# Kernel optimization log

Measured on AMD Instinct MI355X. Metric: run time of the kernel, lower is better.

The kernel has to match this reference:

```python
import jax, jax.numpy as jnp
import numpy as np

E = 50000      # entity_total
R = 100        # relation_total
DIM = 128      # config.dim
M = 10         # max_context_num
M1 = M + 1
T = 2 * R + 2  # entity_gcn_weight rows (2R+1) + appended zero row
B = 1024


def setup_inputs() -> dict:
    key = jax.random.key(0)
    ks = jax.random.split(key, 40)
    f = jnp.float32
    stdv = 1.0 / np.sqrt(DIM)
    inp = {}
    inp['entity_emb'] = jax.random.normal(ks[0], (E, DIM), f) * 0.05
    inp['relation_emb'] = jax.random.normal(ks[1], (R, DIM), f) * 0.05
    ec = jax.random.normal(ks[2], (E + 1, DIM), f) * 0.05
    inp['entity_context'] = ec.at[E].set(0.0)   # padding_idx row = 0
    rc = jax.random.normal(ks[3], (R + 1, DIM), f) * 0.05
    inp['relation_context'] = rc.at[R].set(0.0)
    inp['entity_gcn_weight'] = jax.random.uniform(ks[4], (2 * R + 1, DIM, DIM), f, -stdv, stdv)
    inp['relation_gcn_weight'] = jax.random.uniform(ks[5], (DIM, DIM), f, -stdv, stdv)
    inp['gate_entity'] = jax.random.uniform(ks[6], (DIM,), f)
    inp['gate_relation'] = jax.random.uniform(ks[7], (DIM,), f)
    inp['v_ent'] = jax.random.uniform(ks[8], (DIM,), f)
    inp['v_rel'] = jax.random.uniform(ks[9], (DIM,), f)
    inp['pos_h'] = jax.random.randint(ks[10], (B,), 0, E)
    inp['pos_r'] = jax.random.randint(ks[11], (B,), 0, R)
    inp['pos_t'] = jax.random.randint(ks[12], (B,), 0, E)
    inp['neg_h'] = jax.random.randint(ks[13], (B,), 0, E)
    inp['neg_r'] = jax.random.randint(ks[14], (B,), 0, R)
    inp['neg_t'] = jax.random.randint(ks[15], (B,), 0, E)
    inp['ph_adj'] = jax.random.randint(ks[16], (B, M), 0, E + 1)
    inp['pt_adj'] = jax.random.randint(ks[17], (B, M), 0, E + 1)
    inp['nh_adj'] = jax.random.randint(ks[18], (B, M), 0, E + 1)
    inp['nt_adj'] = jax.random.randint(ks[19], (B, M), 0, E + 1)
    inp['pr_adj'] = jax.random.randint(ks[20], (B, M, 2), 0, R + 1)
    inp['nr_adj'] = jax.random.randint(ks[21], (B, M, 2), 0, R + 1)
    inp['ph_R'] = jax.random.randint(ks[22], (B, M1, M1), 0, T)
    inp['pt_R'] = jax.random.randint(ks[23], (B, M1, M1), 0, T)
    inp['nh_R'] = jax.random.randint(ks[24], (B, M1, M1), 0, T)
    inp['nt_R'] = jax.random.randint(ks[25], (B, M1, M1), 0, T)
    inp['ph_nn'] = jax.random.randint(ks[26], (B,), 0, M)
    inp['pt_nn'] = jax.random.randint(ks[27], (B,), 0, M)
    inp['nh_nn'] = jax.random.randint(ks[28], (B,), 0, M)
    inp['nt_nn'] = jax.random.randint(ks[29], (B,), 0, M)
    inp['ph_D'] = jax.random.uniform(ks[30], (B, M1, M1), f)
    inp['pt_D'] = jax.random.uniform(ks[31], (B, M1, M1), f)
    inp['nh_D'] = jax.random.uniform(ks[32], (B, M1, M1), f)
    inp['nt_D'] = jax.random.uniform(ks[33], (B, M1, M1), f)
    inp['pr_A'] = jax.random.normal(ks[34], (B, M1, M1), f)
    inp['nr_A'] = jax.random.normal(ks[35], (B, M1, M1), f)
    return inp


def reference(entity_emb, relation_emb, entity_context, relation_context,
              entity_gcn_weight, relation_gcn_weight, gate_entity, gate_relation,
              v_ent, v_rel,
              pos_h, pos_r, pos_t, neg_h, neg_r, neg_t,
              ph_adj, pt_adj, nh_adj, nt_adj, pr_adj, nr_adj,
              ph_R, pt_R, nh_R, nt_R, ph_nn, pt_nn, nh_nn, nt_nn,
              ph_D, pt_D, nh_D, nt_D, pr_A, nr_A):
    # weight table with trailing zero row (padding relation type T-1)
    Wfull = jnp.concatenate(
        [entity_gcn_weight, jnp.zeros((1, DIM, DIM), entity_gcn_weight.dtype)], axis=0)

    def ent_ctx(vec, adj_idx):
        # center vector + M gathered context vectors -> [B, M1, d]
        return jnp.concatenate([vec[:, None, :], entity_context[adj_idx]], axis=1)

    def rel_ctx(vec, adj_idx):
        # relation context comes in (head,tail) pairs, summed over the 2
        a = relation_context[adj_idx].sum(axis=2)  # [B, M, d]
        return jnp.concatenate([vec[:, None, :], a], axis=1)

    def rgcn(Rt, Dm, nn_, H):
        # vectorized R-GCN: out[b,j] = relu(sum_k D[b,j,k] * H[b,j] @ W[Rt[b,j,k]])
        # restricted to the dynamic (n+1)x(n+1) block via masking.
        j = jnp.arange(M1)
        valid = j[None, :] <= nn_[:, None]                 # [B, M1]
        pair = valid[:, :, None] & valid[:, None, :]       # [B, M1, M1]
        Rm = jnp.where(pair, Rt, T - 1)                    # pad -> zero weight
        Dd = jnp.where(pair, Dm, jnp.zeros((), Dm.dtype))
        # segment-reduce D over relation types: C[b,j,t] = sum_{k: Rm=t} D[b,j,k]
        C = (jax.nn.one_hot(Rm, T, dtype=H.dtype) * Dd[..., None]).sum(axis=2)  # [B,M1,T]
        S = jnp.einsum('bjt,tde->bjde', C, Wfull)          # [B, M1, d, d]
        out = jax.nn.relu(jnp.einsum('bjd,bjde->bje', H, S))
        return jnp.where(valid[..., None], out, jnp.zeros((), out.dtype))

    def gcn_rel(A, H):
        return jax.nn.relu(jnp.einsum('bij,bjd,de->bie', A, H, relation_gcn_weight))

    def subgraph(o, adj, v):
        # attention over context rows, then weighted sum
        tmp = jax.nn.relu(adj * o[:, None, :])             # [B, M1, d]
        alpha = jax.nn.softmax(tmp @ v, axis=1)            # [B, M1]
        return jnp.sum(alpha[..., None] * adj, axis=1)     # [B, d]

    p_h = entity_emb[pos_h]; p_t = entity_emb[pos_t]; p_r = relation_emb[pos_r]
    n_h = entity_emb[neg_h]; n_t = entity_emb[neg_t]; n_r = relation_emb[neg_r]

    ph_v = rgcn(ph_R, ph_D, ph_nn, ent_ctx(p_h, ph_adj))
    pt_v = rgcn(pt_R, pt_D, pt_nn, ent_ctx(p_t, pt_adj))
    nh_v = rgcn(nh_R, nh_D, nh_nn, ent_ctx(n_h, nh_adj))
    nt_v = rgcn(nt_R, nt_D, nt_nn, ent_ctx(n_t, nt_adj))
    pr_v = gcn_rel(pr_A, rel_ctx(p_r, pr_adj))
    nr_v = gcn_rel(nr_A, rel_ctx(n_r, nr_adj))

    ph_sg = subgraph(p_h, ph_v, v_ent); pt_sg = subgraph(p_t, pt_v, v_ent)
    nh_sg = subgraph(n_h, nh_v, v_ent); nt_sg = subgraph(n_t, nt_v, v_ent)
    pr_sg = subgraph(p_r, pr_v, v_rel); nr_sg = subgraph(n_r, nr_v, v_rel)

    ge = jax.nn.sigmoid(gate_entity)
    gr = jax.nn.sigmoid(gate_relation)
    ph_o = ge * p_h + (1 - ge) * ph_sg
    pt_o = ge * p_t + (1 - ge) * pt_sg
    nh_o = ge * n_h + (1 - ge) * nh_sg
    nt_o = ge * n_t + (1 - ge) * nt_sg
    pr_o = gr * p_r + (1 - gr) * pr_sg
    nr_o = gr * n_r + (1 - gr) * nr_sg

    p_score = jnp.linalg.norm(ph_o + pr_o - pt_o, ord=2, axis=1)
    n_score = jnp.linalg.norm(nh_o + nr_o - nt_o, ord=2, axis=1)
    return (p_score, n_score)
```

## Files before the change

### kernel.cpp

```cpp
#include <hip/hip_runtime.h>
#include <math.h>

#define B_   1024
#define M_   10
#define M1_  11
#define DIM_ 128
#define NW_  201
#define NQUAD_ (4*B_*M1_*M1_)
#define IPB_  64
#define SLOTS_ 2048
#define SCATB_ 242
#define WTILES_ ((NW_+1)*16)
#define MAXCHK_ (NW_ + NQUAD_/IPB_)

typedef __attribute__((ext_vector_type(8))) short bf16x8;
typedef __attribute__((ext_vector_type(4))) float f32x4;

struct GatherPtrs {
    const int* center[4];
    const int* adj[4];
    const int* nn[4];
    const int* Rt[4];
    const float* Dm[4];
};

struct RelPtrs {
    const int* center[2];
    const int* adj2[2];
    const float* A[2];
};

__device__ __forceinline__ unsigned short f2bf(float f) {
    union { float f; unsigned u; } v; v.f = f;
    const unsigned r = v.u + 0x7FFFu + ((v.u >> 16) & 1u);
    return (unsigned short)(r >> 16);
}

template <int N>
__device__ __forceinline__ void block_reduce_bcast(float (&p)[N], float (*sred)[N],
                                                   int e, float (&sc)[N])
{
    #pragma unroll
    for (int off = 32; off; off >>= 1)
        #pragma unroll
        for (int i = 0; i < N; ++i) p[i] += __shfl_xor(p[i], off, 64);
    __syncthreads();
    if ((e & 63) == 0) {
        #pragma unroll
        for (int i = 0; i < N; ++i) sred[e >> 6][i] = p[i];
    }
    __syncthreads();
    #pragma unroll
    for (int i = 0; i < N; ++i) sc[i] = sred[0][i] + sred[1][i];
}

__device__ __forceinline__ float attn_pool(const float (&vm)[M1_], float o, float ve,
                                           float (*sred)[M1_], int e)
{
    float p[M1_];
    #pragma unroll
    for (int j = 0; j < M1_; ++j) p[j] = fmaxf(vm[j] * o, 0.f) * ve;
    float sc[M1_];
    block_reduce_bcast<M1_>(p, sred, e, sc);
    float mx = sc[0];
    #pragma unroll
    for (int j = 1; j < M1_; ++j) mx = fmaxf(mx, sc[j]);
    float s = 0.f, ex[M1_];
    #pragma unroll
    for (int j = 0; j < M1_; ++j) { ex[j] = expf(sc[j] - mx); s += ex[j]; }
    const float inv = 1.f / s;
    float sg = 0.f;
    #pragma unroll
    for (int j = 0; j < M1_; ++j) sg += ex[j] * inv * vm[j];
    return sg;
}

__global__ __launch_bounds__(256)
void prep_kernel(GatherPtrs gp,
                 const float* __restrict__ W, const float* __restrict__ Wr,
                 unsigned short* __restrict__ WT,
                 int* __restrict__ cursor,
                 int2* __restrict__ itemsEQ, float* __restrict__ itemsD)
{
    __shared__ int lh[NW_];
    __shared__ int lbase[NW_];
    __shared__ float tile[32][33];
    const int tid = threadIdx.x;
    const int bid = blockIdx.x;

    if (bid < SCATB_) {
        if (tid < NW_) lh[tid] = 0;
        __syncthreads();
        int rr[8], rk[8], ei[8], qv[8];
        float dv[8];
        #pragma unroll
        for (int s = 0; s < 8; ++s) {
            const int idx = bid * 2048 + s * 256 + tid;
            const int c = idx / (B_ * M1_ * M1_);
            const int rem = idx % (B_ * M1_ * M1_);
            const int b = rem / (M1_ * M1_);
            const int jk = rem % (M1_ * M1_);
            const int j = jk / M1_, k = jk % M1_;
            const int n = gp.nn[c][b];
            rr[s] = -1;
            if (j <= n && k <= n) {
                const int r = gp.Rt[c][rem];
                if (r < NW_) {
                    rr[s] = r;
                    rk[s] = atomicAdd(&lh[r], 1);
                    const int eidx = (j == 0) ? gp.center[c][b]
                                              : gp.adj[c][b * M_ + (j - 1)];
                    ei[s] = (eidx << 1) | (j != 0);
                    qv[s] = idx;
                    dv[s] = gp.Dm[c][rem];
                }
            }
        }
        __syncthreads();
        if (tid < NW_) lbase[tid] = lh[tid] ? atomicAdd(&cursor[tid], lh[tid]) : 0;
        __syncthreads();
        #pragma unroll
        for (int s = 0; s < 8; ++s)
            if (rr[s] >= 0) {
                const int slot = lbase[rr[s]] + rk[s];
                if (slot < SLOTS_) {
                    itemsEQ[rr[s] * SLOTS_ + slot] = make_int2(ei[s], qv[s]);
                    itemsD[rr[s] * SLOTS_ + slot] = dv[s];
                }
            }
    } else {
        const int tl = bid - SCATB_;
        const int t = tl >> 4, sub = tl & 15;
        const int bd = (sub >> 2) * 32, be = (sub & 3) * 32;
        const float* Ws = (t < NW_) ? (W + (size_t)t * DIM_ * DIM_) : Wr;
        unsigned short* Wd = WT + (size_t)t * DIM_ * DIM_;
        const int tx = tid & 31, ty = tid >> 5;
        #pragma unroll
        for (int r = 0; r < 32; r += 8)
            tile[r + ty][tx] = Ws[(bd + r + ty) * DIM_ + be + tx];
        __syncthreads();
        #pragma unroll
        for (int r = 0; r < 32; r += 8)
            Wd[(be + r + ty) * DIM_ + bd + tx] = f2bf(tile[tx][r + ty]);
    }
}

__global__ __launch_bounds__(256)
void chunkbuild_kernel(const int* __restrict__ cursor,
                       int* __restrict__ chunkTab, int* __restrict__ nchunks)
{
    __shared__ int nch[NW_];
    __shared__ int bs[NW_ + 1];
    const int t = threadIdx.x;
    if (t < NW_) {
        const int cnt = min(cursor[t], SLOTS_);
        nch[t] = (cnt + IPB_ - 1) >> 6;
    }
    __syncthreads();
    if (t == 0) {
        int acc = 0;
        for (int i = 0; i < NW_; ++i) { bs[i] = acc; acc += nch[i]; }
        bs[NW_] = acc;
        nchunks[0] = acc;
    }
    __syncthreads();
    if (t < NW_)
        for (int c = 0; c < nch[t]; ++c) chunkTab[bs[t] + c] = (t << 16) | c;
}

template <bool FAST>
__global__ __launch_bounds__(256)
void rgcn_gemm(const float* __restrict__ ent_emb,
               const float* __restrict__ ent_ctx,
               const unsigned short* __restrict__ WT,
               const int2* __restrict__ itemsEQ,
               const float* __restrict__ itemsD,
               const int* __restrict__ cursor,
               const int* __restrict__ chunkTab,
               const int* __restrict__ nchunks,
               _Float16* __restrict__ partial,
               float* __restrict__ vent)
{
    __shared__ unsigned short sH[IPB_ * DIM_];
    __shared__ int sQ[IPB_];
    __shared__ float sD[IPB_];

    const int bid = blockIdx.x;
    if (bid >= nchunks[0]) return;
    const int ent = chunkTab[bid];
    const int t = ent >> 16, ch = ent & 0xffff;
    const int cnt = min(cursor[t], SLOTS_);
    const int istart = ch * IPB_;
    const int nItems = min(IPB_, cnt - istart);
    const int tid = threadIdx.x;
    const int2* eqBase = itemsEQ + t * SLOTS_ + istart;

    #pragma unroll
    for (int it4 = 0; it4 < 4; ++it4) {
        const int m = it4 * 256 + tid;
        const int it = m >> 4, chd = m & 15;
        uint4 pkd;
        if (it < nItems) {
            const int2 eq = eqBase[it];
            if (chd == 0) {
                sQ[it] = eq.y;
                sD[it] = itemsD[t * SLOTS_ + istart + it];
            }
            const float* srow = (eq.x & 1)
                ? ent_ctx + (size_t)(eq.x >> 1) * DIM_
                : ent_emb + (size_t)(eq.x >> 1) * DIM_;
            const float4* s4 = (const float4*)srow + chd * 2;
            const float4 v0 = s4[0], v1 = s4[1];
            pkd.x = (unsigned)f2bf(v0.x) | ((unsigned)f2bf(v0.y) << 16);
            pkd.y = (unsigned)f2bf(v0.z) | ((unsigned)f2bf(v0.w) << 16);
            pkd.z = (unsigned)f2bf(v1.x) | ((unsigned)f2bf(v1.y) << 16);
            pkd.w = (unsigned)f2bf(v1.z) | ((unsigned)f2bf(v1.w) << 16);
        } else {
            if (chd == 0) { sQ[it] = -1; sD[it] = 0.f; }
            pkd.x = pkd.y = pkd.z = pkd.w = 0u;
        }
        const int so = it * 256 + ((chd * 16) ^ ((it & 7) << 4));
        *reinterpret_cast<uint4*>(reinterpret_cast<char*>(sH) + so) = pkd;
    }
    __syncthreads();

    const int w = tid >> 6, l = tid & 63;
    const int lr = l & 15, lk = l >> 4;
    const unsigned short* Wp = WT + (size_t)t * DIM_ * DIM_;
    const f32x4 z = {0.f, 0.f, 0.f, 0.f};
    f32x4 acc[4][2];
    #pragma unroll
    for (int mi = 0; mi < 4; ++mi) { acc[mi][0] = z; acc[mi][1] = z; }

    #pragma unroll
    for (int kb = 0; kb < 4; ++kb) {
        const int o = kb * 64 + lk * 16;
        bf16x8 af[4], bfr[2];
        #pragma unroll
        for (int ni = 0; ni < 2; ++ni) {
            const int row = (2 * w + ni) * 16 + lr;
            bfr[ni] = *reinterpret_cast<const bf16x8*>(Wp + (size_t)row * DIM_ + kb * 32 + lk * 8);
        }
        #pragma unroll
        for (int mi = 0; mi < 4; ++mi) {
            const int row = mi * 16 + lr;
            af[mi] = *reinterpret_cast<const bf16x8*>(
                reinterpret_cast<const char*>(sH) + row * 256 + (o ^ ((row & 7) << 4)));
        }
        #pragma unroll
        for (int mi = 0; mi < 4; ++mi)
            #pragma unroll
            for (int ni = 0; ni < 2; ++ni)
                acc[mi][ni] = __builtin_amdgcn_mfma_f32_16x16x32_bf16(
                    af[mi], bfr[ni], acc[mi][ni], 0, 0, 0);
    }

    #pragma unroll
    for (int mi = 0; mi < 4; ++mi) {
        #pragma unroll
        for (int jj = 0; jj < 4; ++jj) {
            const int it = mi * 16 + lk * 4 + jj;
            const int q = sQ[it];
            if (q >= 0) {
                const float d = sD[it];
                #pragma unroll
                for (int ni = 0; ni < 2; ++ni) {
                    const int col = (2 * w + ni) * 16 + lr;
                    const float val = acc[mi][ni][jj] * d;
                    if (FAST) {
                        partial[(size_t)q * DIM_ + col] = (_Float16)val;
                    } else {
                        unsafeAtomicAdd(vent + (size_t)(q / M1_) * DIM_ + col, val);
                    }
                }
            }
        }
    }
}

template <bool FAST>
__global__ __launch_bounds__(128)
void pool_kernel(GatherPtrs gp, RelPtrs rp,
                 const float* __restrict__ ent_emb,
                 const float* __restrict__ rel_emb,
                 const float* __restrict__ rel_ctx,
                 const unsigned short* __restrict__ WT,
                 const float* __restrict__ v_ent,
                 const float* __restrict__ v_rel,
                 const _Float16* __restrict__ partial,
                 const float* __restrict__ vent,
                 float* __restrict__ sgbuf)
{
    __shared__ float sred[2][M1_];
    const int b = blockIdx.x, c = blockIdx.y, e = threadIdx.x;

    if (c < 4) {
        __shared__ int sRt[M1_ * M1_];
        const int n = gp.nn[c][b];
        if (FAST && e < M1_ * M1_) sRt[e] = gp.Rt[c][b * (M1_ * M1_) + e];
        __syncthreads();

        const float o = ent_emb[(size_t)gp.center[c][b] * DIM_ + e];
        float vm[M1_];
        if (FAST) {
            #pragma unroll
            for (int j = 0; j < M1_; ++j) {
                float s = 0.f;
                if (j <= n) {
                    const int base = (c * B_ + b) * (M1_ * M1_) + j * M1_;
                    #pragma unroll
                    for (int k = 0; k < M1_; ++k) {
                        const float v = (float)partial[(size_t)(base + k) * DIM_ + e];
                        s += (k <= n && sRt[j * M1_ + k] < NW_) ? v : 0.f;
                    }
                    s = fmaxf(s, 0.f);
                }
                vm[j] = s;
            }
        } else {
            const float* vmat = vent + ((size_t)(c * B_ + b)) * M1_ * DIM_;
            #pragma unroll
            for (int j = 0; j < M1_; ++j)
                vm[j] = (j <= n) ? fmaxf(vmat[j * DIM_ + e], 0.f) : 0.f;
        }
        const float sg = attn_pool(vm, o, v_ent[e], sred, e);
        sgbuf[((size_t)c * B_ + b) * DIM_ + e] = sg;
    } else {
        __shared__ float sA[M1_ * M1_];
        __shared__ unsigned short sAH[16 * DIM_];
        __shared__ float sOut[M1_][DIM_];
        const int cse = c - 4;
        const int* adj2 = rp.adj2[cse];

        float h[M1_];
        const float o = rel_emb[(size_t)rp.center[cse][b] * DIM_ + e];
        h[0] = o;
        #pragma unroll
        for (int j = 1; j < M1_; ++j) {
            const int a0 = adj2[((b * M_) + (j - 1)) * 2 + 0];
            const int a1 = adj2[((b * M_) + (j - 1)) * 2 + 1];
            h[j] = rel_ctx[(size_t)a0 * DIM_ + e] + rel_ctx[(size_t)a1 * DIM_ + e];
        }
        if (e < M1_ * M1_) sA[e] = rp.A[cse][b * (M1_ * M1_) + e];
        __syncthreads();

        #pragma unroll
        for (int i = 0; i < M1_; ++i) {
            float s = 0.f;
            #pragma unroll
            for (int jj = 0; jj < M1_; ++jj) s += sA[i * M1_ + jj] * h[jj];
            *reinterpret_cast<unsigned short*>(
                reinterpret_cast<char*>(sAH) + i * 256 + ((2 * e) ^ ((i & 7) << 4))) = f2bf(s);
        }
        #pragma unroll
        for (int i = M1_; i < 16; ++i)
            *reinterpret_cast<unsigned short*>(
                reinterpret_cast<char*>(sAH) + i * 256 + ((2 * e) ^ ((i & 7) << 4))) = 0;
        __syncthreads();

        const int w = e >> 6, l = e & 63;
        const int lr = l & 15, lk = l >> 4;
        const unsigned short* WrT = WT + (size_t)NW_ * DIM_ * DIM_;
        const f32x4 z = {0.f, 0.f, 0.f, 0.f};
        f32x4 acc[4] = {z, z, z, z};
        #pragma unroll
        for (int kb = 0; kb < 4; ++kb) {
            const bf16x8 af = *reinterpret_cast<const bf16x8*>(
                reinterpret_cast<const char*>(sAH) + lr * 256 + ((kb * 64 + lk * 16) ^ ((lr & 7) << 4)));
            #pragma unroll
            for (int ni = 0; ni < 4; ++ni) {
                const int cb = w * 4 + ni;
                const bf16x8 bfr = *reinterpret_cast<const bf16x8*>(
                    WrT + (size_t)(cb * 16 + lr) * DIM_ + kb * 32 + lk * 8);
                acc[ni] = __builtin_amdgcn_mfma_f32_16x16x32_bf16(af, bfr, acc[ni], 0, 0, 0);
            }
        }
        #pragma unroll
        for (int ni = 0; ni < 4; ++ni) {
            const int col = (w * 4 + ni) * 16 + lr;
            #pragma unroll
            for (int jj = 0; jj < 4; ++jj) {
                const int i = lk * 4 + jj;
                if (i < M1_) sOut[i][col] = fmaxf(acc[ni][jj], 0.f);
            }
        }
        __syncthreads();

        float vm[M1_];
        #pragma unroll
        for (int i = 0; i < M1_; ++i) vm[i] = sOut[i][e];
        const float sg = attn_pool(vm, o, v_rel[e], sred, e);
        sgbuf[((size_t)c * B_ + b) * DIM_ + e] = sg;
    }
}

__global__ __launch_bounds__(128)
void score_kernel(GatherPtrs gp,
                  const float* __restrict__ ent_emb,
                  const float* __restrict__ rel_emb,
                  const int* __restrict__ pos_r, const int* __restrict__ neg_r,
                  const float* __restrict__ gate_e, const float* __restrict__ gate_r,
                  const float* __restrict__ sgbuf,
                  float* __restrict__ out)
{
    __shared__ float sred[2][2];
    const int b = blockIdx.x, e = threadIdx.x;

    float cvec[4], osg[4];
    #pragma unroll
    for (int c = 0; c < 4; ++c) {
        cvec[c] = ent_emb[(size_t)gp.center[c][b] * DIM_ + e];
        osg[c] = sgbuf[((size_t)c * B_ + b) * DIM_ + e];
    }
    const float rvec0 = rel_emb[(size_t)pos_r[b] * DIM_ + e];
    const float rvec1 = rel_emb[(size_t)neg_r[b] * DIM_ + e];
    const float rsg0 = sgbuf[((size_t)4 * B_ + b) * DIM_ + e];
    const float rsg1 = sgbuf[((size_t)5 * B_ + b) * DIM_ + e];

    const float ge = 1.f / (1.f + expf(-gate_e[e]));
    const float gr = 1.f / (1.f + expf(-gate_r[e]));
    const float ph_o = ge * cvec[0] + (1.f - ge) * osg[0];
    const float pt_o = ge * cvec[1] + (1.f - ge) * osg[1];
    const float nh_o = ge * cvec[2] + (1.f - ge) * osg[2];
    const float nt_o = ge * cvec[3] + (1.f - ge) * osg[3];
    const float pr_o = gr * rvec0 + (1.f - gr) * rsg0;
    const float nr_o = gr * rvec1 + (1.f - gr) * rsg1;

    const float pv = ph_o + pr_o - pt_o;
    const float nv = nh_o + nr_o - nt_o;
    float p2[2] = { pv * pv, nv * nv };
    float sc2[2];
    block_reduce_bcast<2>(p2, sred, e, sc2);
    if (e == 0) { out[b] = sqrtf(sc2[0]); out[B_ + b] = sqrtf(sc2[1]); }
}

extern "C" void kernel_launch(void* const* d_in, const int* in_sizes, int n_in,
                              void* d_out, int out_size, void* d_ws, size_t ws_size,
                              hipStream_t stream)
{
    const float* entity_emb   = (const float*)d_in[0];
    const float* relation_emb = (const float*)d_in[1];
    const float* entity_ctx   = (const float*)d_in[2];
    const float* relation_ctx = (const float*)d_in[3];
    const float* egw          = (const float*)d_in[4];
    const float* rgw          = (const float*)d_in[5];
    const float* gate_e       = (const float*)d_in[6];
    const float* gate_r       = (const float*)d_in[7];
    const float* v_ent        = (const float*)d_in[8];
    const float* v_rel        = (const float*)d_in[9];
    const int* pos_h = (const int*)d_in[10];
    const int* pos_r = (const int*)d_in[11];
    const int* pos_t = (const int*)d_in[12];
    const int* neg_h = (const int*)d_in[13];
    const int* neg_r = (const int*)d_in[14];
    const int* neg_t = (const int*)d_in[15];
    const int* ph_adj = (const int*)d_in[16];
    const int* pt_adj = (const int*)d_in[17];
    const int* nh_adj = (const int*)d_in[18];
    const int* nt_adj = (const int*)d_in[19];
    const int* pr_adj = (const int*)d_in[20];
    const int* nr_adj = (const int*)d_in[21];
    const int* ph_R = (const int*)d_in[22];
    const int* pt_R = (const int*)d_in[23];
    const int* nh_R = (const int*)d_in[24];
    const int* nt_R = (const int*)d_in[25];
    const int* ph_nn = (const int*)d_in[26];
    const int* pt_nn = (const int*)d_in[27];
    const int* nh_nn = (const int*)d_in[28];
    const int* nt_nn = (const int*)d_in[29];
    const float* ph_D = (const float*)d_in[30];
    const float* pt_D = (const float*)d_in[31];
    const float* nh_D = (const float*)d_in[32];
    const float* nt_D = (const float*)d_in[33];
    const float* pr_A = (const float*)d_in[34];
    const float* nr_A = (const float*)d_in[35];

    GatherPtrs gp;
    gp.center[0] = pos_h; gp.center[1] = pos_t; gp.center[2] = neg_h; gp.center[3] = neg_t;
    gp.adj[0] = ph_adj; gp.adj[1] = pt_adj; gp.adj[2] = nh_adj; gp.adj[3] = nt_adj;
    gp.nn[0] = ph_nn; gp.nn[1] = pt_nn; gp.nn[2] = nh_nn; gp.nn[3] = nt_nn;
    gp.Rt[0] = ph_R; gp.Rt[1] = pt_R; gp.Rt[2] = nh_R; gp.Rt[3] = nt_R;
    gp.Dm[0] = ph_D; gp.Dm[1] = pt_D; gp.Dm[2] = nh_D; gp.Dm[3] = nt_D;

    RelPtrs rp;
    rp.center[0] = pos_r; rp.center[1] = neg_r;
    rp.adj2[0] = pr_adj; rp.adj2[1] = nr_adj;
    rp.A[0] = pr_A; rp.A[1] = nr_A;

    char* wsb = (char*)d_ws;
    const size_t partialBytes = (size_t)NQUAD_ * DIM_ * 2;
    const size_t eqBytes      = (size_t)NW_ * SLOTS_ * 8;
    const size_t dBytes       = (size_t)NW_ * SLOTS_ * 4;
    const size_t metaBytes    = 65536;
    const size_t wtBytes      = (size_t)(NW_ + 1) * DIM_ * DIM_ * 2;
    const size_t sgBytes      = (size_t)6 * B_ * DIM_ * 4;
    const size_t fastNeed = partialBytes + eqBytes + dBytes + metaBytes + wtBytes;
    const bool fast = (ws_size >= fastNeed);

    if (fast) {
        _Float16* partial = (_Float16*)wsb;
        int2* itemsEQ = (int2*)(wsb + partialBytes);
        float* itemsD = (float*)(wsb + partialBytes + eqBytes);
        char* meta    = wsb + partialBytes + eqBytes + dBytes;
        int* cursor   = (int*)meta;
        int* nchunks  = (int*)(meta + 1024);
        int* chunkTab = (int*)(meta + 2048);
        char* wsg = wsb + partialBytes + eqBytes + dBytes + metaBytes;
        unsigned short* WT = (unsigned short*)wsg;
        float* sgbuf       = (float*)wsg;

        hipMemsetAsync(cursor, 0, 1024, stream);
        prep_kernel<<<dim3(SCATB_ + WTILES_), dim3(256), 0, stream>>>(
            gp, egw, rgw, WT, cursor, itemsEQ, itemsD);
        chunkbuild_kernel<<<dim3(1), dim3(256), 0, stream>>>(cursor, chunkTab, nchunks);
        rgcn_gemm<true><<<dim3(MAXCHK_), dim3(256), 0, stream>>>(
            entity_emb, entity_ctx, WT, itemsEQ, itemsD, cursor, chunkTab, nchunks,
            partial, nullptr);
        pool_kernel<true><<<dim3(B_, 6), dim3(128), 0, stream>>>(
            gp, rp, entity_emb, relation_emb, relation_ctx, WT,
            v_ent, v_rel, partial, nullptr, sgbuf);
        score_kernel<<<dim3(B_), dim3(128), 0, stream>>>(
            gp, entity_emb, relation_emb, pos_r, neg_r, gate_e, gate_r, sgbuf, (float*)d_out);
    } else {
        float* vent = (float*)wsb;
        const size_t ventBytes = (size_t)4 * B_ * M1_ * DIM_ * 4;
        unsigned short* WT = (unsigned short*)(wsb + ventBytes);
        float* sgbuf  = (float*)(wsb + ventBytes + wtBytes);
        int2* itemsEQ = (int2*)(wsb + ventBytes + wtBytes + sgBytes);
        float* itemsD = (float*)(wsb + ventBytes + wtBytes + sgBytes + eqBytes);
        char* meta    = wsb + ventBytes + wtBytes + sgBytes + eqBytes + dBytes;
        int* cursor   = (int*)meta;
        int* nchunks  = (int*)(meta + 1024);
        int* chunkTab = (int*)(meta + 2048);

        hipMemsetAsync(vent, 0, ventBytes, stream);
        hipMemsetAsync(cursor, 0, 1024, stream);
        prep_kernel<<<dim3(SCATB_ + WTILES_), dim3(256), 0, stream>>>(
            gp, egw, rgw, WT, cursor, itemsEQ, itemsD);
        chunkbuild_kernel<<<dim3(1), dim3(256), 0, stream>>>(cursor, chunkTab, nchunks);
        rgcn_gemm<false><<<dim3(MAXCHK_), dim3(256), 0, stream>>>(
            entity_emb, entity_ctx, WT, itemsEQ, itemsD, cursor, chunkTab, nchunks,
            nullptr, vent);
        pool_kernel<false><<<dim3(B_, 6), dim3(128), 0, stream>>>(
            gp, rp, entity_emb, relation_emb, relation_ctx, WT,
            v_ent, v_rel, nullptr, vent, sgbuf);
        score_kernel<<<dim3(B_), dim3(128), 0, stream>>>(
            gp, entity_emb, relation_emb, pos_r, neg_r, gate_e, gate_r, sgbuf, (float*)d_out);
    }
}
```

Before: 95.78 us.

## Fuse chunk build into prep via last-block pattern and merge pool with score

Removes the single-block chunkbuild launch. The last scatter block of prep_kernel, detected through an atomic done counter placed in the memset region, now builds the chunk table. pool_kernel and score_kernel are merged into one 768-thread epi_kernel per batch row, so the sg intermediate stays in shared memory and the global sgbuf round trip plus one launch go away. The cost is a larger block with more shared memory, which may lower occupancy, plus a threadfence and atomic in the scatter blocks.

New measurement: 151.1 us. +57.8%, slower.

```diff
diff --git a/kernel.cpp b/kernel.cpp
--- a/kernel.cpp
+++ b/kernel.cpp
@@ -36,55 +36,20 @@
     return (unsigned short)(r >> 16);
 }
 
-template <int N>
-__device__ __forceinline__ void block_reduce_bcast(float (&p)[N], float (*sred)[N],
-                                                   int e, float (&sc)[N])
-{
-    #pragma unroll
-    for (int off = 32; off; off >>= 1)
-        #pragma unroll
-        for (int i = 0; i < N; ++i) p[i] += __shfl_xor(p[i], off, 64);
-    __syncthreads();
-    if ((e & 63) == 0) {
-        #pragma unroll
-        for (int i = 0; i < N; ++i) sred[e >> 6][i] = p[i];
-    }
-    __syncthreads();
-    #pragma unroll
-    for (int i = 0; i < N; ++i) sc[i] = sred[0][i] + sred[1][i];
-}
-
-__device__ __forceinline__ float attn_pool(const float (&vm)[M1_], float o, float ve,
-                                           float (*sred)[M1_], int e)
-{
-    float p[M1_];
-    #pragma unroll
-    for (int j = 0; j < M1_; ++j) p[j] = fmaxf(vm[j] * o, 0.f) * ve;
-    float sc[M1_];
-    block_reduce_bcast<M1_>(p, sred, e, sc);
-    float mx = sc[0];
-    #pragma unroll
-    for (int j = 1; j < M1_; ++j) mx = fmaxf(mx, sc[j]);
-    float s = 0.f, ex[M1_];
-    #pragma unroll
-    for (int j = 0; j < M1_; ++j) { ex[j] = expf(sc[j] - mx); s += ex[j]; }
-    const float inv = 1.f / s;
-    float sg = 0.f;
-    #pragma unroll
-    for (int j = 0; j < M1_; ++j) sg += ex[j] * inv * vm[j];
-    return sg;
-}
-
 __global__ __launch_bounds__(256)
 void prep_kernel(GatherPtrs gp,
                  const float* __restrict__ W, const float* __restrict__ Wr,
                  unsigned short* __restrict__ WT,
-                 int* __restrict__ cursor,
-                 int2* __restrict__ itemsEQ, float* __restrict__ itemsD)
+                 int* __restrict__ cursor, int* __restrict__ done,
+                 int2* __restrict__ itemsEQ, float* __restrict__ itemsD,
+                 int* __restrict__ chunkTab, int* __restrict__ nchunks)
 {
     __shared__ int lh[NW_];
     __shared__ int lbase[NW_];
     __shared__ float tile[32][33];
+    __shared__ int sLast;
+    __shared__ int nchS[NW_];
+    __shared__ int bsS[NW_ + 1];
     const int tid = threadIdx.x;
     const int bid = blockIdx.x;
 
@@ -128,6 +93,26 @@
                     itemsD[rr[s] * SLOTS_ + slot] = dv[s];
                 }
             }
+        __threadfence();
+        __syncthreads();
+        if (tid == 0) sLast = (atomicAdd(done, 1) == SCATB_ - 1);
+        __syncthreads();
+        if (sLast) {
+            if (tid < NW_) {
+                const int cnt = min(atomicAdd(&cursor[tid], 0), SLOTS_);
+                nchS[tid] = (cnt + IPB_ - 1) >> 6;
+            }
+            __syncthreads();
+            if (tid == 0) {
+                int acc = 0;
+                for (int i = 0; i < NW_; ++i) { bsS[i] = acc; acc += nchS[i]; }
+                nchunks[0] = acc;
+            }
+            __syncthreads();
+            if (tid < NW_)
+                for (int c = 0; c < nchS[tid]; ++c)
+                    chunkTab[bsS[tid] + c] = (tid << 16) | c;
+        }
     } else {
         const int tl = bid - SCATB_;
         const int t = tl >> 4, sub = tl & 15;
@@ -143,29 +128,6 @@
         for (int r = 0; r < 32; r += 8)
             Wd[(be + r + ty) * DIM_ + bd + tx] = f2bf(tile[tx][r + ty]);
     }
-}
-
-__global__ __launch_bounds__(256)
-void chunkbuild_kernel(const int* __restrict__ cursor,
-                       int* __restrict__ chunkTab, int* __restrict__ nchunks)
-{
-    __shared__ int nch[NW_];
-    __shared__ int bs[NW_ + 1];
-    const int t = threadIdx.x;
-    if (t < NW_) {
-        const int cnt = min(cursor[t], SLOTS_);
-        nch[t] = (cnt + IPB_ - 1) >> 6;
-    }
-    __syncthreads();
-    if (t == 0) {
-        int acc = 0;
-        for (int i = 0; i < NW_; ++i) { bs[i] = acc; acc += nch[i]; }
-        bs[NW_] = acc;
-        nchunks[0] = acc;
-    }
-    __syncthreads();
-    if (t < NW_)
-        for (int c = 0; c < nch[t]; ++c) chunkTab[bs[t] + c] = (t << 16) | c;
 }
 
 template <bool FAST>
@@ -279,85 +241,98 @@
 }
 
 template <bool FAST>
-__global__ __launch_bounds__(128)
-void pool_kernel(GatherPtrs gp, RelPtrs rp,
-                 const float* __restrict__ ent_emb,
-                 const float* __restrict__ rel_emb,
-                 const float* __restrict__ rel_ctx,
-                 const unsigned short* __restrict__ WT,
-                 const float* __restrict__ v_ent,
-                 const float* __restrict__ v_rel,
-                 const _Float16* __restrict__ partial,
-                 const float* __restrict__ vent,
-                 float* __restrict__ sgbuf)
+__global__ __launch_bounds__(768)
+void epi_kernel(GatherPtrs gp, RelPtrs rp,
+                const float* __restrict__ ent_emb,
+                const float* __restrict__ rel_emb,
+                const float* __restrict__ rel_ctx,
+                const unsigned short* __restrict__ WT,
+                const float* __restrict__ v_ent,
+                const float* __restrict__ v_rel,
+                const float* __restrict__ gate_e,
+                const float* __restrict__ gate_r,
+                const _Float16* __restrict__ partial,
+                const float* __restrict__ vent,
+                float* __restrict__ out)
 {
-    __shared__ float sred[2][M1_];
-    const int b = blockIdx.x, c = blockIdx.y, e = threadIdx.x;
-
-    if (c < 4) {
-        __shared__ int sRt[M1_ * M1_];
-        const int n = gp.nn[c][b];
-        if (FAST && e < M1_ * M1_) sRt[e] = gp.Rt[c][b * (M1_ * M1_) + e];
-        __syncthreads();
-
-        const float o = ent_emb[(size_t)gp.center[c][b] * DIM_ + e];
-        float vm[M1_];
+    __shared__ float sSG[6][DIM_];
+    __shared__ float sred[6][2][M1_];
+    __shared__ int   sRt[4][M1_ * M1_];
+    __shared__ float sA[2][M1_ * M1_];
+    __shared__ unsigned short sAH[2][16 * DIM_];
+    __shared__ float sOut[2][M1_][DIM_];
+    __shared__ float sredS[12][2];
+
+    const int b = blockIdx.x;
+    const int g = threadIdx.x >> 7;
+    const int e = threadIdx.x & 127;
+
+    float vm[M1_];
+    float h[M1_];
+    float o, vkey;
+
+    if (g < 4) {
+        if (FAST && e < M1_ * M1_) sRt[g][e] = gp.Rt[g][b * (M1_ * M1_) + e];
+        o = ent_emb[(size_t)gp.center[g][b] * DIM_ + e];
+        vkey = v_ent[e];
+    } else {
+        const int cse = g - 4;
+        const int* adj2 = rp.adj2[cse];
+        o = rel_emb[(size_t)rp.center[cse][b] * DIM_ + e];
+        h[0] = o;
+        #pragma unroll
+        for (int j = 1; j < M1_; ++j) {
+            const int a0 = adj2[((b * M_) + (j - 1)) * 2 + 0];
+            const int a1 = adj2[((b * M_) + (j - 1)) * 2 + 1];
+            h[j] = rel_ctx[(size_t)a0 * DIM_ + e] + rel_ctx[(size_t)a1 * DIM_ + e];
+        }
+        if (e < M1_ * M1_) sA[cse][e] = rp.A[cse][b * (M1_ * M1_) + e];
+        vkey = v_rel[e];
+    }
+    __syncthreads();
+
+    if (g >= 4) {
+        const int cse = g - 4;
+        #pragma unroll
+        for (int i = 0; i < M1_; ++i) {
+            float s = 0.f;
+            #pragma unroll
+            for (int jj = 0; jj < M1_; ++jj) s += sA[cse][i * M1_ + jj] * h[jj];
+            *reinterpret_cast<unsigned short*>(
+                reinterpret_cast<char*>(sAH[cse]) + i * 256 + ((2 * e) ^ ((i & 7) << 4))) = f2bf(s);
+        }
+        #pragma unroll
+        for (int i = M1_; i < 16; ++i)
+            *reinterpret_cast<unsigned short*>(
+                reinterpret_cast<char*>(sAH[cse]) + i * 256 + ((2 * e) ^ ((i & 7) << 4))) = 0;
+    }
+    __syncthreads();
+
+    if (g < 4) {
+        const int n = gp.nn[g][b];
         if (FAST) {
             #pragma unroll
             for (int j = 0; j < M1_; ++j) {
                 float s = 0.f;
                 if (j <= n) {
-                    const int base = (c * B_ + b) * (M1_ * M1_) + j * M1_;
+                    const int base = (g * B_ + b) * (M1_ * M1_) + j * M1_;
                     #pragma unroll
                     for (int k = 0; k < M1_; ++k) {
                         const float v = (float)partial[(size_t)(base + k) * DIM_ + e];
-                        s += (k <= n && sRt[j * M1_ + k] < NW_) ? v : 0.f;
+                        s += (k <= n && sRt[g][j * M1_ + k] < NW_) ? v : 0.f;
                     }
                     s = fmaxf(s, 0.f);
                 }
                 vm[j] = s;
             }
         } else {
-            const float* vmat = vent + ((size_t)(c * B_ + b)) * M1_ * DIM_;
+            const float* vmat = vent + ((size_t)(g * B_ + b)) * M1_ * DIM_;
             #pragma unroll
             for (int j = 0; j < M1_; ++j)
                 vm[j] = (j <= n) ? fmaxf(vmat[j * DIM_ + e], 0.f) : 0.f;
         }
-        const float sg = attn_pool(vm, o, v_ent[e], sred, e);
-        sgbuf[((size_t)c * B_ + b) * DIM_ + e] = sg;
     } else {
-        __shared__ float sA[M1_ * M1_];
-        __shared__ unsigned short sAH[16 * DIM_];
-        __shared__ float sOut[M1_][DIM_];
-        const int cse = c - 4;
-        const int* adj2 = rp.adj2[cse];
-
-        float h[M1_];
-        const float o = rel_emb[(size_t)rp.center[cse][b] * DIM_ + e];
-        h[0] = o;
-        #pragma unroll
-        for (int j = 1; j < M1_; ++j) {
-            const int a0 = adj2[((b * M_) + (j - 1)) * 2 + 0];
-            const int a1 = adj2[((b * M_) + (j - 1)) * 2 + 1];
-            h[j] = rel_ctx[(size_t)a0 * DIM_ + e] + rel_ctx[(size_t)a1 * DIM_ + e];
-        }
-        if (e < M1_ * M1_) sA[e] = rp.A[cse][b * (M1_ * M1_) + e];
-        __syncthreads();
-
-        #pragma unroll
-        for (int i = 0; i < M1_; ++i) {
-            float s = 0.f;
-            #pragma unroll
-            for (int jj = 0; jj < M1_; ++jj) s += sA[i * M1_ + jj] * h[jj];
-            *reinterpret_cast<unsigned short*>(
-                reinterpret_cast<char*>(sAH) + i * 256 + ((2 * e) ^ ((i & 7) << 4))) = f2bf(s);
-        }
-        #pragma unroll
-        for (int i = M1_; i < 16; ++i)
-            *reinterpret_cast<unsigned short*>(
-                reinterpret_cast<char*>(sAH) + i * 256 + ((2 * e) ^ ((i & 7) << 4))) = 0;
-        __syncthreads();
-
+        const int cse = g - 4;
         const int w = e >> 6, l = e & 63;
         const int lr = l & 15, lk = l >> 4;
         const unsigned short* WrT = WT + (size_t)NW_ * DIM_ * DIM_;
@@ -366,7 +341,7 @@
         #pragma unroll
         for (int kb = 0; kb < 4; ++kb) {
             const bf16x8 af = *reinterpret_cast<const bf16x8*>(
-                reinterpret_cast<const char*>(sAH) + lr * 256 + ((kb * 64 + lk * 16) ^ ((lr & 7) << 4)));
+                reinterpret_cast<const char*>(sAH[cse]) + lr * 256 + ((kb * 64 + lk * 16) ^ ((lr & 7) << 4)));
             #pragma unroll
             for (int ni = 0; ni < 4; ++ni) {
                 const int cb = w * 4 + ni;
@@ -381,57 +356,80 @@
             #pragma unroll
             for (int jj = 0; jj < 4; ++jj) {
                 const int i = lk * 4 + jj;
-                if (i < M1_) sOut[i][col] = fmaxf(acc[ni][jj], 0.f);
-            }
-        }
-        __syncthreads();
-
-        float vm[M1_];
-        #pragma unroll
-        for (int i = 0; i < M1_; ++i) vm[i] = sOut[i][e];
-        const float sg = attn_pool(vm, o, v_rel[e], sred, e);
-        sgbuf[((size_t)c * B_ + b) * DIM_ + e] = sg;
-    }
-}
-
-__global__ __launch_bounds__(128)
-void score_kernel(GatherPtrs gp,
-                  const float* __restrict__ ent_emb,
-                  const float* __restrict__ rel_emb,
-                  const int* __restrict__ pos_r, const int* __restrict__ neg_r,
-                  const float* __restrict__ gate_e, const float* __restrict__ gate_r,
-                  const float* __restrict__ sgbuf,
-                  float* __restrict__ out)
-{
-    __shared__ float sred[2][2];
-    const int b = blockIdx.x, e = threadIdx.x;
-
-    float cvec[4], osg[4];
-    #pragma unroll
-    for (int c = 0; c < 4; ++c) {
-        cvec[c] = ent_emb[(size_t)gp.center[c][b] * DIM_ + e];
-        osg[c] = sgbuf[((size_t)c * B_ + b) * DIM_ + e];
-    }
-    const float rvec0 = rel_emb[(size_t)pos_r[b] * DIM_ + e];
-    const float rvec1 = rel_emb[(size_t)neg_r[b] * DIM_ + e];
-    const float rsg0 = sgbuf[((size_t)4 * B_ + b) * DIM_ + e];
-    const float rsg1 = sgbuf[((size_t)5 * B_ + b) * DIM_ + e];
-
-    const float ge = 1.f / (1.f + expf(-gate_e[e]));
-    const float gr = 1.f / (1.f + expf(-gate_r[e]));
-    const float ph_o = ge * cvec[0] + (1.f - ge) * osg[0];
-    const float pt_o = ge * cvec[1] + (1.f - ge) * osg[1];
-    const float nh_o = ge * cvec[2] + (1.f - ge) * osg[2];
-    const float nt_o = ge * cvec[3] + (1.f - ge) * osg[3];
-    const float pr_o = gr * rvec0 + (1.f - gr) * rsg0;
-    const float nr_o = gr * rvec1 + (1.f - gr) * rsg1;
-
-    const float pv = ph_o + pr_o - pt_o;
-    const float nv = nh_o + nr_o - nt_o;
-    float p2[2] = { pv * pv, nv * nv };
-    float sc2[2];
-    block_reduce_bcast<2>(p2, sred, e, sc2);
-    if (e == 0) { out[b] = sqrtf(sc2[0]); out[B_ + b] = sqrtf(sc2[1]); }
+                if (i < M1_) sOut[cse][i][col] = fmaxf(acc[ni][jj], 0.f);
+            }
+        }
+    }
+    __syncthreads();
+
+    if (g >= 4) {
+        #pragma unroll
+        for (int i = 0; i < M1_; ++i) vm[i] = sOut[g - 4][i][e];
+    }
+    float p[M1_];
+    #pragma unroll
+    for (int j = 0; j < M1_; ++j) p[j] = fmaxf(vm[j] * o, 0.f) * vkey;
+    #pragma unroll
+    for (int off = 32; off; off >>= 1)
+        #pragma unroll
+        for (int i = 0; i < M1_; ++i) p[i] += __shfl_xor(p[i], off, 64);
+    if ((e & 63) == 0) {
+        #pragma unroll
+        for (int i = 0; i < M1_; ++i) sred[g][e >> 6][i] = p[i];
+    }
+    __syncthreads();
+    {
+        float sc[M1_];
+        #pragma unroll
+        for (int i = 0; i < M1_; ++i) sc[i] = sred[g][0][i] + sred[g][1][i];
+        float mx = sc[0];
+        #pragma unroll
+        for (int j = 1; j < M1_; ++j) mx = fmaxf(mx, sc[j]);
+        float s = 0.f, ex[M1_];
+        #pragma unroll
+        for (int j = 0; j < M1_; ++j) { ex[j] = expf(sc[j] - mx); s += ex[j]; }
+        const float inv = 1.f / s;
+        float sg = 0.f;
+        #pragma unroll
+        for (int j = 0; j < M1_; ++j) sg += ex[j] * inv * vm[j];
+        sSG[g][e] = sg;
+    }
+    __syncthreads();
+
+    float p2a = 0.f, p2b = 0.f;
+    if (g == 0) {
+        float cvec[4];
+        #pragma unroll
+        for (int c = 0; c < 4; ++c)
+            cvec[c] = ent_emb[(size_t)gp.center[c][b] * DIM_ + e];
+        const float rvec0 = rel_emb[(size_t)rp.center[0][b] * DIM_ + e];
+        const float rvec1 = rel_emb[(size_t)rp.center[1][b] * DIM_ + e];
+        const float ge = 1.f / (1.f + expf(-gate_e[e]));
+        const float gr = 1.f / (1.f + expf(-gate_r[e]));
+        const float ph_o = ge * cvec[0] + (1.f - ge) * sSG[0][e];
+        const float pt_o = ge * cvec[1] + (1.f - ge) * sSG[1][e];
+        const float nh_o = ge * cvec[2] + (1.f - ge) * sSG[2][e];
+        const float nt_o = ge * cvec[3] + (1.f - ge) * sSG[3][e];
+        const float pr_o = gr * rvec0 + (1.f - gr) * sSG[4][e];
+        const float nr_o = gr * rvec1 + (1.f - gr) * sSG[5][e];
+        const float pv = ph_o + pr_o - pt_o;
+        const float nv = nh_o + nr_o - nt_o;
+        p2a = pv * pv; p2b = nv * nv;
+    }
+    #pragma unroll
+    for (int off = 32; off; off >>= 1) {
+        p2a += __shfl_xor(p2a, off, 64);
+        p2b += __shfl_xor(p2b, off, 64);
+    }
+    const int wv = threadIdx.x >> 6;
+    if ((threadIdx.x & 63) == 0) { sredS[wv][0] = p2a; sredS[wv][1] = p2b; }
+    __syncthreads();
+    if (threadIdx.x == 0) {
+        float sa = 0.f, sb = 0.f;
+        #pragma unroll
+        for (int w2 = 0; w2 < 12; ++w2) { sa += sredS[w2][0]; sb += sredS[w2][1]; }
+        out[b] = sqrtf(sa); out[B_ + b] = sqrtf(sb);
+    }
 }
 
 extern "C" void kernel_launch(void* const* d_in, const int* in_sizes, int n_in,
@@ -493,7 +491,6 @@
     const size_t dBytes       = (size_t)NW_ * SLOTS_ * 4;
     const size_t metaBytes    = 65536;
     const size_t wtBytes      = (size_t)(NW_ + 1) * DIM_ * DIM_ * 2;
-    const size_t sgBytes      = (size_t)6 * B_ * DIM_ * 4;
     const size_t fastNeed = partialBytes + eqBytes + dBytes + metaBytes + wtBytes;
     const bool fast = (ws_size >= fastNeed);
 
@@ -503,48 +500,41 @@
         float* itemsD = (float*)(wsb + partialBytes + eqBytes);
         char* meta    = wsb + partialBytes + eqBytes + dBytes;
         int* cursor   = (int*)meta;
+        int* done     = (int*)(meta + 960);
         int* nchunks  = (int*)(meta + 1024);
         int* chunkTab = (int*)(meta + 2048);
-        char* wsg = wsb + partialBytes + eqBytes + dBytes + metaBytes;
-        unsigned short* WT = (unsigned short*)wsg;
-        float* sgbuf       = (float*)wsg;
+        unsigned short* WT = (unsigned short*)(wsb + partialBytes + eqBytes + dBytes + metaBytes);
 
         hipMemsetAsync(cursor, 0, 1024, stream);
         prep_kernel<<<dim3(SCATB_ + WTILES_), dim3(256), 0, stream>>>(
-            gp, egw, rgw, WT, cursor, itemsEQ, itemsD);
-        chunkbuild_kernel<<<dim3(1), dim3(256), 0, stream>>>(cursor, chunkTab, nchunks);
+            gp, egw, rgw, WT, cursor, done, itemsEQ, itemsD, chunkTab, nchunks);
         rgcn_gemm<true><<<dim3(MAXCHK_), dim3(256), 0, stream>>>(
             entity_emb, entity_ctx, WT, itemsEQ, itemsD, cursor, chunkTab, nchunks,
             partial, nullptr);
-        pool_kernel<true><<<dim3(B_, 6), dim3(128), 0, stream>>>(
+        epi_kernel<true><<<dim3(B_), dim3(768), 0, stream>>>(
             gp, rp, entity_emb, relation_emb, relation_ctx, WT,
-            v_ent, v_rel, partial, nullptr, sgbuf);
-        score_kernel<<<dim3(B_), dim3(128), 0, stream>>>(
-            gp, entity_emb, relation_emb, pos_r, neg_r, gate_e, gate_r, sgbuf, (float*)d_out);
+            v_ent, v_rel, gate_e, gate_r, partial, nullptr, (float*)d_out);
     } else {
         float* vent = (float*)wsb;
         const size_t ventBytes = (size_t)4 * B_ * M1_ * DIM_ * 4;
         unsigned short* WT = (unsigned short*)(wsb + ventBytes);
-        float* sgbuf  = (float*)(wsb + ventBytes + wtBytes);
-        int2* itemsEQ = (int2*)(wsb + ventBytes + wtBytes + sgBytes);
-        float* itemsD = (float*)(wsb + ventBytes + wtBytes + sgBytes + eqBytes);
-        char* meta    = wsb + ventBytes + wtBytes + sgBytes + eqBytes + dBytes;
+        int2* itemsEQ = (int2*)(wsb + ventBytes + wtBytes);
+        float* itemsD = (float*)(wsb + ventBytes + wtBytes + eqBytes);
+        char* meta    = wsb + ventBytes + wtBytes + eqBytes + dBytes;
         int* cursor   = (int*)meta;
+        int* done     = (int*)(meta + 960);
         int* nchunks  = (int*)(meta + 1024);
         int* chunkTab = (int*)(meta + 2048);
 
         hipMemsetAsync(vent, 0, ventBytes, stream);
         hipMemsetAsync(cursor, 0, 1024, stream);
         prep_kernel<<<dim3(SCATB_ + WTILES_), dim3(256), 0, stream>>>(
-            gp, egw, rgw, WT, cursor, itemsEQ, itemsD);
-        chunkbuild_kernel<<<dim3(1), dim3(256), 0, stream>>>(cursor, chunkTab, nchunks);
+            gp, egw, rgw, WT, cursor, done, itemsEQ, itemsD, chunkTab, nchunks);
         rgcn_gemm<false><<<dim3(MAXCHK_), dim3(256), 0, stream>>>(
             entity_emb, entity_ctx, WT, itemsEQ, itemsD, cursor, chunkTab, nchunks,
             nullptr, vent);
-        pool_kernel<false><<<dim3(B_, 6), dim3(128), 0, stream>>>(
+        epi_kernel<false><<<dim3(B_), dim3(768), 0, stream>>>(
             gp, rp, entity_emb, relation_emb, relation_ctx, WT,
-            v_ent, v_rel, nullptr, vent, sgbuf);
-        score_kernel<<<dim3(B_), dim3(128), 0, stream>>>(
-            gp, entity_emb, relation_emb, pos_r, neg_r, gate_e, gate_r, sgbuf, (float*)d_out);
+            v_ent, v_rel, gate_e, gate_r, nullptr, vent, (float*)d_out);
     }
 }
```
